# Kernel tuning notes

Measured on AMD Instinct MI355X. Metric: run time of the kernel, lower is better.

Reference implementation:

```python
import jax, jax.numpy as jnp
import numpy as np

K = 5000  # module's self.dim

def setup_inputs() -> dict:
    key = jax.random.key(0)
    x = jax.random.normal(key, (50_000_000,), dtype=jnp.float32)
    return {"x": x}

def reference(x):
    # top-k values and their indices (lax.top_k returns them sorted by value,
    # but the subsequent argsort over indices restores original-index order,
    # matching torch.topk(sorted=False) + argsort + gather exactly)
    vals, idx = jax.lax.top_k(x, K)          # [K], [K]
    order = jnp.argsort(idx)                 # permutation restoring input order
    return vals[order]                       # [K] order-preserving top-k subset
```

## Files before the change

kernel.cpp:

```cpp
#include <hip/hip_runtime.h>

#define K_TOP 5000
#define NBIN 2048
#define CAND_LDS 1024
#define NB_BUCKET 4096
#define TARGET_SAMPLED 94u

__device__ __forceinline__ unsigned f2key(float f) {
    unsigned u = __float_as_uint(f);
    return (u & 0x80000000u) ? ~u : (u | 0x80000000u);
}
__device__ __forceinline__ float key2f(unsigned k) {
    unsigned u = (k & 0x80000000u) ? (k ^ 0x80000000u) : ~k;
    return __uint_as_float(u);
}

__global__ __launch_bounds__(256) void k_sample(const float4* __restrict__ x4, long n4,
                                                unsigned* __restrict__ hist) {
    __shared__ unsigned lh[NBIN];
    for (int i = threadIdx.x; i < NBIN; i += 256) lh[i] = 0;
    __syncthreads();
    int wave = threadIdx.x >> 6;
    int lane = threadIdx.x & 63;
    long gw = (long)blockIdx.x * 4 + wave;
    long totW = (long)gridDim.x * 4;
    long nChunk = (n4 + 8191) / 8192;
    for (long c = gw; c < nChunk; c += totW) {
        long i = c * 8192 + lane;
        if (i < n4) {
            float4 v = x4[i];
            atomicAdd(&lh[f2key(v.x) >> 21], 1u);
            atomicAdd(&lh[f2key(v.y) >> 21], 1u);
            atomicAdd(&lh[f2key(v.z) >> 21], 1u);
            atomicAdd(&lh[f2key(v.w) >> 21], 1u);
        }
    }
    __syncthreads();
    for (int i = threadIdx.x; i < NBIN; i += 256) {
        unsigned c = lh[i];
        if (c) atomicAdd(&hist[i], c);
    }
}

__global__ __launch_bounds__(256) void k_findbin(const unsigned* __restrict__ hist,
                                                 unsigned* __restrict__ ctrl) {
    __shared__ unsigned lh[NBIN];
    __shared__ unsigned gs[64];
    for (int i = threadIdx.x; i < NBIN; i += 256) lh[i] = hist[i];
    __syncthreads();
    int t = threadIdx.x;
    if (t < 64) {
        unsigned s = 0;
        for (int j = 0; j < 32; j++) s += lh[t * 32 + j];
        gs[t] = s;
    }
    __syncthreads();
    if (t == 0) {
        unsigned cum = 0;
        int g = 63;
        for (; g > 0; g--) { if (cum + gs[g] >= TARGET_SAMPLED) break; cum += gs[g]; }
        int b = g * 32 + 31;
        for (; b > g * 32; b--) { if (cum + lh[b] >= TARGET_SAMPLED) break; cum += lh[b]; }
        ctrl[1] = ((unsigned)b) << 21;
    }
}

__global__ __launch_bounds__(256) void k_compact(const float4* __restrict__ x4, long n4,
                                                 long n, const float* __restrict__ x,
                                                 unsigned* __restrict__ ctrl,
                                                 unsigned* __restrict__ candKey,
                                                 unsigned* __restrict__ candIdx,
                                                 unsigned capC) {
    __shared__ unsigned sKey[CAND_LDS], sIdx[CAND_LDS];
    __shared__ unsigned sCnt, sBase;
    if (threadIdx.x == 0) sCnt = 0;
    __syncthreads();
    unsigned L = ctrl[1];
    unsigned* candCount = &ctrl[0];

    int tail = (int)(n & 3);
    if (blockIdx.x == 0 && threadIdx.x < tail) {
        unsigned k = f2key(x[n4 * 4 + threadIdx.x]);
        if (k >= L) {
            unsigned p = atomicAdd(&sCnt, 1u);
            if (p < CAND_LDS) { sKey[p] = k; sIdx[p] = (unsigned)(n4 * 4 + threadIdx.x); }
            else {
                unsigned q = atomicAdd(candCount, 1u);
                if (q < capC) { candKey[q] = k; candIdx[q] = (unsigned)(n4 * 4 + threadIdx.x); }
            }
        }
    }

    long tiles = (n4 + 1023) >> 10;
    for (long tile = blockIdx.x; tile < tiles; tile += gridDim.x) {
        long base = tile << 10;
        long i0 = base + threadIdx.x;
        long i1 = i0 + 256, i2 = i0 + 512, i3 = i0 + 768;
        bool in0 = i0 < n4, in1 = i1 < n4, in2 = i2 < n4, in3 = i3 < n4;
        float4 v0, v1, v2, v3;
        if (in0) v0 = x4[i0];
        if (in1) v1 = x4[i1];
        if (in2) v2 = x4[i2];
        if (in3) v3 = x4[i3];
#define PROC(vv, inb, ii)                                                            \
        if (inb) {                                                                   \
            unsigned kk, bb = (unsigned)((ii) * 4);                                  \
            kk = f2key((vv).x);                                                      \
            if (kk >= L) { unsigned p = atomicAdd(&sCnt, 1u);                        \
                if (p < CAND_LDS) { sKey[p] = kk; sIdx[p] = bb; }                    \
                else { unsigned q = atomicAdd(candCount, 1u);                        \
                       if (q < capC) { candKey[q] = kk; candIdx[q] = bb; } } }       \
            kk = f2key((vv).y);                                                      \
            if (kk >= L) { unsigned p = atomicAdd(&sCnt, 1u);                        \
                if (p < CAND_LDS) { sKey[p] = kk; sIdx[p] = bb + 1; }                \
                else { unsigned q = atomicAdd(candCount, 1u);                        \
                       if (q < capC) { candKey[q] = kk; candIdx[q] = bb + 1; } } }   \
            kk = f2key((vv).z);                                                      \
            if (kk >= L) { unsigned p = atomicAdd(&sCnt, 1u);                        \
                if (p < CAND_LDS) { sKey[p] = kk; sIdx[p] = bb + 2; }                \
                else { unsigned q = atomicAdd(candCount, 1u);                        \
                       if (q < capC) { candKey[q] = kk; candIdx[q] = bb + 2; } } }   \
            kk = f2key((vv).w);                                                      \
            if (kk >= L) { unsigned p = atomicAdd(&sCnt, 1u);                        \
                if (p < CAND_LDS) { sKey[p] = kk; sIdx[p] = bb + 3; }                \
                else { unsigned q = atomicAdd(candCount, 1u);                        \
                       if (q < capC) { candKey[q] = kk; candIdx[q] = bb + 3; } } }   \
        }
        PROC(v0, in0, i0)
        PROC(v1, in1, i1)
        PROC(v2, in2, i2)
        PROC(v3, in3, i3)
#undef PROC
    }
    __syncthreads();
    unsigned cnt = sCnt; if (cnt > CAND_LDS) cnt = CAND_LDS;
    if (threadIdx.x == 0) sBase = atomicAdd(candCount, cnt);
    __syncthreads();
    unsigned bp = sBase;
    for (unsigned i = threadIdx.x; i < cnt; i += 256) {
        unsigned q = bp + i;
        if (q < capC) { candKey[q] = sKey[i]; candIdx[q] = sIdx[i]; }
    }
}

__global__ __launch_bounds__(1024) void k_final(const unsigned* __restrict__ candKey,
                                                const unsigned* __restrict__ candIdx,
                                                unsigned* __restrict__ ctrl, unsigned capC,
                                                unsigned* __restrict__ selKey,
                                                unsigned* __restrict__ selIdx,
                                                unsigned* __restrict__ selKeyS,
                                                unsigned* __restrict__ selIdxS,
                                                float* __restrict__ out, long n, int bshift) {
    __shared__ unsigned h[NB_BUCKET * 2];
    __shared__ unsigned part[1024];
    __shared__ unsigned part2[32];
    __shared__ unsigned res[2];
    __shared__ unsigned sScalar;
    const int t = threadIdx.x;
    unsigned Nc = ctrl[0]; if (Nc > capC) Nc = capC;
    unsigned L = ctrl[1];

    unsigned mk = 0;
    for (unsigned i = t; i < Nc; i += 1024) { unsigned k = candKey[i]; if (k > mk) mk = k; }
    part[t] = mk;
    __syncthreads();
    if (t < 32) { unsigned m = 0; for (int j = 0; j < 32; j++) { unsigned v = part[t * 32 + j]; if (v > m) m = v; } part2[t] = m; }
    __syncthreads();
    if (t == 0) { unsigned m = 0; for (int j = 0; j < 32; j++) if (part2[j] > m) m = part2[j]; sScalar = m; }
    __syncthreads();
    unsigned maxK = sScalar;

    unsigned lo = L, target = K_TOP;
    unsigned range = maxK - lo;
    int shift = 0;
    while ((range >> shift) >= NBIN) shift++;
    for (;;) {
        int nb = (int)(range >> shift) + 1;
        for (int i = t; i < nb; i += 1024) h[i] = 0;
        __syncthreads();
        for (unsigned i = t; i < Nc; i += 1024) {
            unsigned d = candKey[i] - lo;
            if (d <= range) atomicAdd(&h[d >> shift], 1u);
        }
        __syncthreads();
        int ng = (nb + 31) >> 5;
        if (t < ng) {
            unsigned s = 0; int b0 = t * 32, e = b0 + 32; if (e > nb) e = nb;
            for (int j = b0; j < e; j++) s += h[j];
            part[t] = s;
        }
        __syncthreads();
        if (t == 0) {
            unsigned cum = 0; int g = ng - 1;
            for (; g > 0; g--) { if (cum + part[g] >= target) break; cum += part[g]; }
            int hi2 = g * 32 + 31; if (hi2 > nb - 1) hi2 = nb - 1;
            int b = hi2;
            for (; b > g * 32; b--) { if (cum + h[b] >= target) break; cum += h[b]; }
            res[0] = (unsigned)b; res[1] = target - cum;
        }
        __syncthreads();
        lo += res[0] << shift; target = res[1];
        if (shift == 0) break;
        range = (1u << shift) - 1;
        shift = (shift > 11) ? shift - 11 : 0;
    }
    unsigned T = lo, R = target;

    if (t == 0) sScalar = 0;
    __syncthreads();
    for (unsigned i = t; i < Nc; i += 1024)
        if (candKey[i] == T) atomicAdd(&sScalar, 1u);
    __syncthreads();
    unsigned cntEq = sScalar;
    unsigned idxCut = 0xFFFFFFFFu;
    if (cntEq != R) {
        unsigned lo2 = 0, tgt = R;
        unsigned range2 = (unsigned)(n - 1);
        int sh = 0;
        while ((range2 >> sh) >= NBIN) sh++;
        for (;;) {
            int nb = (int)(range2 >> sh) + 1;
            for (int i = t; i < nb; i += 1024) h[i] = 0;
            __syncthreads();
            for (unsigned i = t; i < Nc; i += 1024)
                if (candKey[i] == T) {
                    unsigned d = candIdx[i] - lo2;
                    if (d <= range2) atomicAdd(&h[d >> sh], 1u);
                }
            __syncthreads();
            int ng = (nb + 31) >> 5;
            if (t < ng) {
                unsigned s = 0; int b0 = t * 32, e = b0 + 32; if (e > nb) e = nb;
                for (int j = b0; j < e; j++) s += h[j];
                part[t] = s;
            }
            __syncthreads();
            if (t == 0) {
                unsigned cum = 0; int g = 0;
                for (; g < ng - 1; g++) { if (cum + part[g] >= tgt) break; cum += part[g]; }
                int b = g * 32; int hi2 = g * 32 + 31; if (hi2 > nb - 1) hi2 = nb - 1;
                for (; b < hi2; b++) { if (cum + h[b] >= tgt) break; cum += h[b]; }
                res[0] = (unsigned)b; res[1] = tgt - cum;
            }
            __syncthreads();
            lo2 += res[0] << sh; tgt = res[1];
            if (sh == 0) break;
            range2 = (1u << sh) - 1;
            sh = (sh > 11) ? sh - 11 : 0;
        }
        idxCut = lo2;
    }
    __syncthreads();

    for (int i = t; i < NB_BUCKET; i += 1024) h[i] = 0;
    if (t == 0) sScalar = 0;
    __syncthreads();
    for (unsigned i = t; i < Nc; i += 1024) {
        unsigned k = candKey[i]; unsigned id = candIdx[i];
        if (k > T || (k == T && id <= idxCut)) {
            unsigned p = atomicAdd(&sScalar, 1u);
            if (p < K_TOP) {
                selKey[p] = k; selIdx[p] = id;
                atomicAdd(&h[id >> bshift], 1u);
            }
        }
    }
    __syncthreads();
    unsigned nSel = sScalar; if (nSel > K_TOP) nSel = K_TOP;

    unsigned* bc = h;
    unsigned* bs = h + NB_BUCKET;
    { unsigned s = 0; for (int j = 0; j < 4; j++) s += bc[t * 4 + j]; part[t] = s; }
    __syncthreads();
    if (t < 32) { unsigned s = 0; for (int j = 0; j < 32; j++) s += part[t * 32 + j]; part2[t] = s; }
    __syncthreads();
    if (t == 0) { unsigned run = 0; for (int j = 0; j < 32; j++) { unsigned v = part2[j]; part2[j] = run; run += v; } }
    __syncthreads();
    if (t < 32) { unsigned run = part2[t]; for (int j = 0; j < 32; j++) { int id2 = t * 32 + j; unsigned v = part[id2]; part[id2] = run; run += v; } }
    __syncthreads();
    { unsigned run = part[t]; for (int j = 0; j < 4; j++) { bs[t * 4 + j] = run; run += bc[t * 4 + j]; } }
    __syncthreads();

    for (unsigned g = t; g < nSel; g += 1024) {
        unsigned id = selIdx[g];
        unsigned b = id >> bshift;
        unsigned p = atomicAdd(&bs[b], 1u);
        if (p < K_TOP) { selKeyS[p] = selKey[g]; selIdxS[p] = id; }
    }
    __syncthreads();

    for (int j = 0; j < 4; j++) {
        int b = t * 4 + j;
        unsigned cnt = bc[b];
        if (!cnt) continue;
        unsigned s = bs[b] - cnt;
        for (unsigned i = 0; i < cnt; i++) {
            unsigned mi = i, mv = selIdxS[s + i];
            for (unsigned q = i + 1; q < cnt; q++) {
                unsigned v = selIdxS[s + q];
                if (v < mv) { mv = v; mi = q; }
            }
            if (mi != i) {
                unsigned ti = selIdxS[s + i]; selIdxS[s + i] = selIdxS[s + mi]; selIdxS[s + mi] = ti;
                unsigned tk = selKeyS[s + i]; selKeyS[s + i] = selKeyS[s + mi]; selKeyS[s + mi] = tk;
            }
            out[s + i] = key2f(selKeyS[s + i]);
        }
    }
}

extern "C" void kernel_launch(void* const* d_in, const int* in_sizes, int n_in,
                              void* d_out, int out_size, void* d_ws, size_t ws_size,
                              hipStream_t stream) {
    const float* x = (const float*)d_in[0];
    long n = in_sizes[0];
    float* out = (float*)d_out;
    unsigned* w = (unsigned*)d_ws;

    unsigned* hist    = w;
    unsigned* ctrl    = w + 2048;
    unsigned* selKey  = w + 2056;
    unsigned* selIdx  = w + 7056;
    unsigned* selKeyS = w + 12056;
    unsigned* selIdxS = w + 17056;
    const size_t CAND_BASE = 24576;
    size_t words = ws_size / 4;
    unsigned capC = 0;
    if (words > CAND_BASE + 64) {
        size_t c = (words - CAND_BASE) / 2;
        if (c > (size_t)(4u << 20)) c = (size_t)(4u << 20);
        capC = (unsigned)c;
    }
    unsigned* candKey = w + CAND_BASE;
    unsigned* candIdx = candKey + capC;

    int bshift = 0;
    while (((n - 1) >> bshift) >= NB_BUCKET) bshift++;

    hipMemsetAsync(d_ws, 0, 2056u * 4u + 32u, stream);

    long n4 = n / 4;
    k_sample<<<256, 256, 0, stream>>>((const float4*)x, n4, hist);
    k_findbin<<<1, 256, 0, stream>>>(hist, ctrl);
    k_compact<<<4096, 256, 0, stream>>>((const float4*)x, n4, n, x, ctrl,
                                        candKey, candIdx, capC);
    k_final<<<1, 1024, 0, stream>>>(candKey, candIdx, ctrl, capC,
                                    selKey, selIdx, selKeyS, selIdxS, out, n, bshift);
}
```

Before: 370.2 us.

## Rewrite compaction with one-tile-per-block grid, wave max early-out, direct global atomics

The compaction kernel now gives each block a single tile of 2048 float4 held in registers, instead of grid-striding over 1024-float4 tiles. It compares in float space, takes a per-thread max and uses a wave-wide __any to skip the candidate path for waves with no values above the threshold. Survivors go straight to global memory through a global atomic counter, dropping the LDS staging buffer and its block-level syncs. The risk is more global atomic contention when candidates are frequent, plus register pressure from holding eight float4 per thread.

```diff
diff --git a/kernel.cpp b/kernel.cpp
--- a/kernel.cpp
+++ b/kernel.cpp
@@ -2,8 +2,8 @@
 
 #define K_TOP 5000
 #define NBIN 2048
-#define CAND_LDS 1024
 #define NB_BUCKET 4096
+#define TILE4 2048
 #define TARGET_SAMPLED 94u
 
 __device__ __forceinline__ unsigned f2key(float f) {
@@ -71,75 +71,44 @@
                                                  unsigned* __restrict__ candKey,
                                                  unsigned* __restrict__ candIdx,
                                                  unsigned capC) {
-    __shared__ unsigned sKey[CAND_LDS], sIdx[CAND_LDS];
-    __shared__ unsigned sCnt, sBase;
-    if (threadIdx.x == 0) sCnt = 0;
-    __syncthreads();
     unsigned L = ctrl[1];
-    unsigned* candCount = &ctrl[0];
-
-    int tail = (int)(n & 3);
-    if (blockIdx.x == 0 && threadIdx.x < tail) {
-        unsigned k = f2key(x[n4 * 4 + threadIdx.x]);
-        if (k >= L) {
-            unsigned p = atomicAdd(&sCnt, 1u);
-            if (p < CAND_LDS) { sKey[p] = k; sIdx[p] = (unsigned)(n4 * 4 + threadIdx.x); }
-            else {
-                unsigned q = atomicAdd(candCount, 1u);
-                if (q < capC) { candKey[q] = k; candIdx[q] = (unsigned)(n4 * 4 + threadIdx.x); }
-            }
-        }
-    }
-
-    long tiles = (n4 + 1023) >> 10;
-    for (long tile = blockIdx.x; tile < tiles; tile += gridDim.x) {
-        long base = tile << 10;
-        long i0 = base + threadIdx.x;
-        long i1 = i0 + 256, i2 = i0 + 512, i3 = i0 + 768;
-        bool in0 = i0 < n4, in1 = i1 < n4, in2 = i2 < n4, in3 = i3 < n4;
-        float4 v0, v1, v2, v3;
-        if (in0) v0 = x4[i0];
-        if (in1) v1 = x4[i1];
-        if (in2) v2 = x4[i2];
-        if (in3) v3 = x4[i3];
-#define PROC(vv, inb, ii)                                                            \
-        if (inb) {                                                                   \
-            unsigned kk, bb = (unsigned)((ii) * 4);                                  \
-            kk = f2key((vv).x);                                                      \
-            if (kk >= L) { unsigned p = atomicAdd(&sCnt, 1u);                        \
-                if (p < CAND_LDS) { sKey[p] = kk; sIdx[p] = bb; }                    \
-                else { unsigned q = atomicAdd(candCount, 1u);                        \
-                       if (q < capC) { candKey[q] = kk; candIdx[q] = bb; } } }       \
-            kk = f2key((vv).y);                                                      \
-            if (kk >= L) { unsigned p = atomicAdd(&sCnt, 1u);                        \
-                if (p < CAND_LDS) { sKey[p] = kk; sIdx[p] = bb + 1; }                \
-                else { unsigned q = atomicAdd(candCount, 1u);                        \
-                       if (q < capC) { candKey[q] = kk; candIdx[q] = bb + 1; } } }   \
-            kk = f2key((vv).z);                                                      \
-            if (kk >= L) { unsigned p = atomicAdd(&sCnt, 1u);                        \
-                if (p < CAND_LDS) { sKey[p] = kk; sIdx[p] = bb + 2; }                \
-                else { unsigned q = atomicAdd(candCount, 1u);                        \
-                       if (q < capC) { candKey[q] = kk; candIdx[q] = bb + 2; } } }   \
-            kk = f2key((vv).w);                                                      \
-            if (kk >= L) { unsigned p = atomicAdd(&sCnt, 1u);                        \
-                if (p < CAND_LDS) { sKey[p] = kk; sIdx[p] = bb + 3; }                \
-                else { unsigned q = atomicAdd(candCount, 1u);                        \
-                       if (q < capC) { candKey[q] = kk; candIdx[q] = bb + 3; } } }   \
-        }
-        PROC(v0, in0, i0)
-        PROC(v1, in1, i1)
-        PROC(v2, in2, i2)
-        PROC(v3, in3, i3)
-#undef PROC
-    }
-    __syncthreads();
-    unsigned cnt = sCnt; if (cnt > CAND_LDS) cnt = CAND_LDS;
-    if (threadIdx.x == 0) sBase = atomicAdd(candCount, cnt);
-    __syncthreads();
-    unsigned bp = sBase;
-    for (unsigned i = threadIdx.x; i < cnt; i += 256) {
-        unsigned q = bp + i;
-        if (q < capC) { candKey[q] = sKey[i]; candIdx[q] = sIdx[i]; }
+    float Lf = key2f(L);
+    long base = (long)blockIdx.x * TILE4 + threadIdx.x;
+    float4 v[8];
+#pragma unroll
+    for (int j = 0; j < 8; j++) {
+        long i = base + (long)j * 256;
+        v[j] = make_float4(-1e38f, -1e38f, -1e38f, -1e38f);
+        if (i < n4) v[j] = x4[i];
+    }
+    float m = -1e38f;
+#pragma unroll
+    for (int j = 0; j < 8; j++)
+        m = fmaxf(m, fmaxf(fmaxf(v[j].x, v[j].y), fmaxf(v[j].z, v[j].w)));
+    if (__any(m >= Lf)) {
+#pragma unroll
+        for (int j = 0; j < 8; j++) {
+            long i = base + (long)j * 256;
+            if (i < n4) {
+                unsigned bb = (unsigned)(i * 4);
+                const float* pv = (const float*)&v[j];
+#pragma unroll
+                for (int c = 0; c < 4; c++) {
+                    float f = pv[c];
+                    if (f >= Lf) {
+                        unsigned p = atomicAdd(&ctrl[0], 1u);
+                        if (p < capC) { candKey[p] = f2key(f); candIdx[p] = bb + (unsigned)c; }
+                    }
+                }
+            }
+        }
+    }
+    if (blockIdx.x == 0 && threadIdx.x < (int)(n & 3)) {
+        float f = x[n4 * 4 + threadIdx.x];
+        if (f >= Lf) {
+            unsigned p = atomicAdd(&ctrl[0], 1u);
+            if (p < capC) { candKey[p] = f2key(f); candIdx[p] = (unsigned)(n4 * 4 + threadIdx.x); }
+        }
     }
 }
 
@@ -340,10 +309,11 @@
     hipMemsetAsync(d_ws, 0, 2056u * 4u + 32u, stream);
 
     long n4 = n / 4;
+    long nBlocks = (n4 + TILE4 - 1) / TILE4;
     k_sample<<<256, 256, 0, stream>>>((const float4*)x, n4, hist);
     k_findbin<<<1, 256, 0, stream>>>(hist, ctrl);
-    k_compact<<<4096, 256, 0, stream>>>((const float4*)x, n4, n, x, ctrl,
-                                        candKey, candIdx, capC);
+    k_compact<<<(int)nBlocks, 256, 0, stream>>>((const float4*)x, n4, n, x, ctrl,
+                                                candKey, candIdx, capC);
     k_final<<<1, 1024, 0, stream>>>(candKey, candIdx, ctrl, capC,
                                     selKey, selIdx, selKeyS, selIdxS, out, n, bshift);
 }
```

Result: slower. 424.0 us (+14.5%).
